# Performance work log

Hardware: AMD Instinct MI355X
Metric: run time of the kernel (lower is better)

Reference implementation:

```python
import jax, jax.numpy as jnp
import numpy as np

D = 256; R = 2; K = 32
N = 32768; NE = 1_000_000; NT = 65_536
BETA_MAX = 5.0; GRAD_CLIP = 1.0; STATE_CLIP = 10.0
DAMP = 0.9999  # update_damping=1.0 clamped to 1-1e-4
EPS = 1e-5


def _xavier(key, din, dout, gain=0.5):
    lim = gain * np.sqrt(6.0 / (din + dout))
    return jax.random.uniform(key, (din, dout), jnp.float32, -lim, lim)


def setup_inputs() -> dict:
    key = jax.random.key(0)
    ks = jax.random.split(key, 16)
    inv_sp1 = float(np.log(np.expm1(1.0)))  # inverse softplus of 1.0
    return {
        "X": jax.random.normal(ks[0], (N, D), jnp.float32),
        "c_2": jax.random.randint(ks[1], (NE,), 0, N, jnp.int32),
        "u_2": jax.random.randint(ks[2], (NE,), 0, N, jnp.int32),
        "c_3": jax.random.randint(ks[3], (NT,), 0, N, jnp.int32),
        "u_3": jax.random.randint(ks[4], (NT,), 0, N, jnp.int32),
        "v_3": jax.random.randint(ks[5], (NT,), 0, N, jnp.int32),
        "t_tau": jax.random.randint(ks[6], (NT,), 0, 2, jnp.int32),
        "step_size": jnp.float32(0.1),
        "ln_gamma": jnp.ones((D,), jnp.float32),
        "ln_beta": jnp.zeros((D,), jnp.float32),
        "W_Q2": _xavier(ks[7], D, D),
        "W_K2": _xavier(ks[8], D, D),
        "W_Q3": _xavier(ks[9], D, R * D),
        "W_K3": _xavier(ks[10], D, R * D),
        "T_tau": 0.02 * jax.random.normal(ks[11], (2, R, D), jnp.float32),
        "W_Qm": _xavier(ks[12], D, D),
        "W_Km": _xavier(ks[13], D, D),
        "B_mem": jax.random.normal(ks[14], (K, D), jnp.float32) / np.sqrt(D),
        "lambda_2": jnp.float32(inv_sp1), "lambda_3": jnp.float32(inv_sp1), "lambda_m": jnp.float32(inv_sp1),
        "beta_2": jnp.float32(inv_sp1), "beta_3": jnp.float32(inv_sp1), "beta_m": jnp.float32(inv_sp1),
    }


def _seg_lse(s, seg, n):
    # logsumexp of s grouped by seg; empty segments contribute 0
    m = jax.ops.segment_max(s, seg, num_segments=n)
    m0 = jnp.where(jnp.isfinite(m), m, 0.0)
    e = jax.ops.segment_sum(jnp.exp(s - m0[seg]), seg, num_segments=n)
    return jnp.where(e > 0, m0 + jnp.log(jnp.maximum(e, 1e-30)), 0.0)


def _energy(X, ln_gamma, ln_beta, W_Q2, W_K2, W_Q3, W_K3, T_tau, W_Qm, W_Km, B_mem,
            lambda_2, lambda_3, lambda_m, beta_2, beta_3, beta_m,
            c_2, u_2, c_3, u_3, v_3, t_tau):
    mu = X.mean(-1, keepdims=True)
    var = ((X - mu) ** 2).mean(-1, keepdims=True)
    G = (X - mu) * jax.lax.rsqrt(var + EPS) * ln_gamma + ln_beta  # [N,D]
    sp = jax.nn.softplus
    lam2, lam3, lamm = sp(lambda_2), sp(lambda_3), sp(lambda_m)
    b2 = jnp.minimum(sp(beta_2), BETA_MAX)
    b3 = jnp.minimum(sp(beta_3), BETA_MAX)
    bm = jnp.minimum(sp(beta_m), BETA_MAX)
    scale = jnp.float32(1.0 / np.sqrt(D))
    # pairwise (order-2) attention energy over edge list
    Q2, K2 = G @ W_Q2, G @ W_K2
    s2 = b2 * scale * jnp.sum(Q2[c_2] * K2[u_2], axis=-1)  # [NE]
    E2 = -(lam2 / b2) * jnp.sum(_seg_lse(s2, c_2, N))
    # motif (order-3) rank-R energy over triangle list with type embedding T_tau
    Q3 = (G @ W_Q3).reshape(N, R, D)
    K3 = (G @ W_K3).reshape(N, R, D)
    s3 = b3 * scale * jnp.sum(Q3[c_3] * K3[u_3] * K3[v_3] * T_tau[t_tau], axis=(1, 2))  # [NT]
    E3 = -(lam3 / b3) * jnp.sum(_seg_lse(s3, c_3, N))
    # memory-slot energy
    Qm, Km = G @ W_Qm, B_mem @ W_Km  # [N,D],[K,D]
    Sm = bm * scale * (Qm @ Km.T)  # [N,K]
    Em = -(lamm / bm) * jnp.sum(jax.nn.logsumexp(Sm, axis=-1))
    return E2 + E3 + Em


def reference(X, c_2, u_2, c_3, u_3, v_3, t_tau, step_size, ln_gamma, ln_beta,
              W_Q2, W_K2, W_Q3, W_K3, T_tau, W_Qm, W_Km, B_mem,
              lambda_2, lambda_3, lambda_m, beta_2, beta_3, beta_m):
    efn = lambda x: _energy(x, ln_gamma, ln_beta, W_Q2, W_K2, W_Q3, W_K3, T_tau,
                            W_Qm, W_Km, B_mem, lambda_2, lambda_3, lambda_m,
                            beta_2, beta_3, beta_m, c_2, u_2, c_3, u_3, v_3, t_tau)
    E, gX = jax.value_and_grad(efn)(X)
    gn = jnp.maximum(jnp.linalg.norm(gX, axis=-1, keepdims=True), 1e-6)
    gX = gX * jnp.minimum(GRAD_CLIP / gn, 1.0)
    X_next = X - step_size * DAMP * gX
    sn = jnp.maximum(jnp.linalg.norm(X_next, axis=-1, keepdims=True), 1e-6)
    X_next = X_next * jnp.minimum(STATE_CLIP / sn, 1.0)
    return X_next, E
```

## Files before the change

kernel.cpp:

```cpp
#include <hip/hip_runtime.h>
#include <math.h>

#define D_ 256
#define KSLOT 32
#define CAP2 128
#define CAP3C 16
#define CAP3I 32
#define NBP 256
#define NBUCK 256
typedef unsigned short ushort_t;
typedef __attribute__((ext_vector_type(8))) short bf16x8;
typedef __attribute__((ext_vector_type(4))) float f32x4;

__device__ __forceinline__ float softplus_f(float x){
  return (x > 20.0f) ? x : log1pf(expf(x));
}
__device__ __forceinline__ float bflo(unsigned u){ return __uint_as_float(u << 16); }
__device__ __forceinline__ float bfhi(unsigned u){ return __uint_as_float(u & 0xFFFF0000u); }
__device__ __forceinline__ ushort_t f2b(float f){
  unsigned u = __float_as_uint(f);
  unsigned r = u + 0x7FFFu + ((u >> 16) & 1u);
  return (ushort_t)(r >> 16);
}
__device__ __forceinline__ unsigned pack2(float a, float b){
  return (unsigned)f2b(a) | ((unsigned)f2b(b) << 16);
}
__device__ __forceinline__ void unpack16(uint4 a, uint4 b, float* f){
  f[0]=bflo(a.x); f[1]=bfhi(a.x); f[2]=bflo(a.y); f[3]=bfhi(a.y);
  f[4]=bflo(a.z); f[5]=bfhi(a.z); f[6]=bflo(a.w); f[7]=bfhi(a.w);
  f[8]=bflo(b.x); f[9]=bfhi(b.x); f[10]=bflo(b.y); f[11]=bfhi(b.y);
  f[12]=bflo(b.z); f[13]=bfhi(b.z); f[14]=bflo(b.w); f[15]=bfhi(b.w);
}
__device__ __forceinline__ float block_reduce_sum(float v, float* sbuf){
  #pragma unroll
  for (int o = 32; o > 0; o >>= 1) v += __shfl_xor(v, o);
  int t = threadIdx.x, wid = t >> 6, lane = t & 63;
  if (lane == 0) sbuf[wid] = v;
  __syncthreads();
  if (t == 0) sbuf[0] = sbuf[0] + sbuf[1] + sbuf[2] + sbuf[3];
  __syncthreads();
  float r = sbuf[0];
  __syncthreads();
  return r;
}

__global__ __launch_bounds__(256) void zerok(float4* __restrict__ p, size_t n4){
  float4 z; z.x = z.y = z.z = z.w = 0.f;
  for (size_t i = (size_t)blockIdx.x * 256 + threadIdx.x; i < n4; i += (size_t)gridDim.x * 256)
    p[i] = z;
}

__global__ __launch_bounds__(256) void ln_fwd(const float* __restrict__ X, const float* __restrict__ gamma,
    const float* __restrict__ beta, ushort_t* __restrict__ Gb, float* __restrict__ mean, float* __restrict__ rstd)
{
  __shared__ float sbuf[8];
  int n = blockIdx.x, t = threadIdx.x;
  size_t idx = (size_t)n * D_ + t;
  float x = X[idx];
  float mu = block_reduce_sum(x, sbuf) * (1.0f / D_);
  float d = x - mu;
  float var = block_reduce_sum(d * d, sbuf) * (1.0f / D_);
  float rs = rsqrtf(var + 1e-5f);
  Gb[idx] = f2b(d * rs * gamma[t] + beta[t]);
  if (t == 0){ mean[n] = mu; rstd[n] = rs; }
}

__global__ __launch_bounds__(256) void wprep_all(const float* __restrict__ W_Q2, const float* __restrict__ W_K2,
    const float* __restrict__ W_Q3, const float* __restrict__ W_K3, const float* __restrict__ W_Qm,
    ushort_t* __restrict__ WtQm, ushort_t* __restrict__ WtF2, ushort_t* __restrict__ WtF3,
    ushort_t* __restrict__ WbQm, ushort_t* __restrict__ Bt2, ushort_t* __restrict__ Bt3)
{
  int idx = blockIdx.x * 256 + threadIdx.x;
  if (idx < 65536){
    int m = idx >> 8, k = idx & 255;
    WtQm[idx] = f2b(W_Qm[k * 256 + m]);
    return;
  }
  idx -= 65536;
  if (idx < 131072){
    int m = idx >> 8, k = idx & 255;
    WtF2[idx] = f2b(m < 256 ? W_Q2[k * 256 + m] : W_K2[k * 256 + (m - 256)]);
    return;
  }
  idx -= 131072;
  if (idx < 262144){
    int m = idx >> 8, k = idx & 255;
    WtF3[idx] = f2b(m < 512 ? W_Q3[k * 512 + m] : W_K3[k * 512 + (m - 512)]);
    return;
  }
  idx -= 262144;
  if (idx < 65536){ WbQm[idx] = f2b(W_Qm[idx]); return; }
  idx -= 65536;
  if (idx < 131072){
    int d = idx >> 9, k = idx & 511;
    Bt2[idx] = f2b(k < 256 ? W_Q2[d * 256 + k] : W_K2[d * 256 + (k - 256)]);
    return;
  }
  idx -= 131072;
  if (idx < 262144){
    int d = idx >> 10, k = idx & 1023;
    Bt3[idx] = f2b(k < 512 ? W_Q3[d * 512 + k] : W_K3[d * 512 + (k - 512)]);
  }
}

template<int OUT_MODE>
__global__ __launch_bounds__(256) void gemm_bt_mfma(const ushort_t* __restrict__ A,
    const ushort_t* __restrict__ Bt, void* __restrict__ C, int K, int M)
{
  __shared__ __align__(16) ushort_t As[128 * 32];
  __shared__ __align__(16) ushort_t Bs[128 * 32];
  int t = threadIdx.x;
  int wave = t >> 6, lane = t & 63;
  int row0 = blockIdx.y * 128;
  int col0 = blockIdx.x * 128;
  int wrow = (wave & 1) * 64;
  int wcol = (wave >> 1) * 64;
  f32x4 acc[4][4];
  #pragma unroll
  for (int i = 0; i < 4; ++i)
    #pragma unroll
    for (int j = 0; j < 4; ++j)
      acc[i][j] = (f32x4){0.f, 0.f, 0.f, 0.f};
  int srow = wave * 32 + (lane >> 2);
  int skoff = (lane & 3) * 8;
  const ushort_t* Ag0 = A + (size_t)(row0 + srow) * K + skoff;
  const ushort_t* Ag1 = A + (size_t)(row0 + srow + 16) * K + skoff;
  const ushort_t* Bg0 = Bt + (size_t)(col0 + srow) * K + skoff;
  const ushort_t* Bg1 = Bt + (size_t)(col0 + srow + 16) * K + skoff;
  ushort_t* Al0 = As + wave * 1024;
  ushort_t* Al1 = As + wave * 1024 + 512;
  ushort_t* Bl0 = Bs + wave * 1024;
  ushort_t* Bl1 = Bs + wave * 1024 + 512;
  int lrow = lane & 15, lk = (lane >> 4) * 8;
  for (int k0 = 0; k0 < K; k0 += 32){
    __syncthreads();
    __builtin_amdgcn_global_load_lds((const __attribute__((address_space(1))) void*)(Ag0 + k0),
                                     (__attribute__((address_space(3))) void*)Al0, 16, 0, 0);
    __builtin_amdgcn_global_load_lds((const __attribute__((address_space(1))) void*)(Ag1 + k0),
                                     (__attribute__((address_space(3))) void*)Al1, 16, 0, 0);
    __builtin_amdgcn_global_load_lds((const __attribute__((address_space(1))) void*)(Bg0 + k0),
                                     (__attribute__((address_space(3))) void*)Bl0, 16, 0, 0);
    __builtin_amdgcn_global_load_lds((const __attribute__((address_space(1))) void*)(Bg1 + k0),
                                     (__attribute__((address_space(3))) void*)Bl1, 16, 0, 0);
    __syncthreads();
    bf16x8 af[4], bf_[4];
    #pragma unroll
    for (int i = 0; i < 4; ++i)
      af[i] = *(const bf16x8*)(As + (wrow + i * 16 + lrow) * 32 + lk);
    #pragma unroll
    for (int j = 0; j < 4; ++j)
      bf_[j] = *(const bf16x8*)(Bs + (wcol + j * 16 + lrow) * 32 + lk);
    #pragma unroll
    for (int i = 0; i < 4; ++i)
      #pragma unroll
      for (int j = 0; j < 4; ++j)
        acc[i][j] = __builtin_amdgcn_mfma_f32_16x16x32_bf16(af[i], bf_[j], acc[i][j], 0, 0, 0);
  }
  int rbase = row0 + wrow + (lane >> 4) * 4;
  int cbase = col0 + wcol + (lane & 15);
  #pragma unroll
  for (int i = 0; i < 4; ++i){
    #pragma unroll
    for (int r = 0; r < 4; ++r){
      size_t rowoff = (size_t)(rbase + i * 16 + r) * M;
      #pragma unroll
      for (int j = 0; j < 4; ++j){
        int col = cbase + j * 16;
        float v = acc[i][j][r];
        if (OUT_MODE == 0)      ((float*)C)[rowoff + col] = v;
        else if (OUT_MODE == 1) ((float*)C)[rowoff + col] += v;
        else                    ((ushort_t*)C)[rowoff + col] = f2b(v);
      }
    }
  }
}

__global__ __launch_bounds__(256) void km_kernel(const float* __restrict__ Bm, const float* __restrict__ W,
    ushort_t* __restrict__ Kmb)
{
  __shared__ float sb[D_];
  int k = blockIdx.x, t = threadIdx.x;
  if (k < KSLOT){
    sb[t] = Bm[(size_t)k * D_ + t];
    __syncthreads();
    float acc = 0.f;
    for (int d = 0; d < D_; ++d) acc += sb[d] * W[(size_t)d * D_ + t];
    Kmb[(size_t)k * D_ + t] = f2b(acc);
  } else {
    Kmb[(size_t)k * D_ + t] = 0;
  }
}

__global__ __launch_bounds__(256) void softmax32(const float* __restrict__ Sm, ushort_t* __restrict__ Pb,
    float* __restrict__ lseM, const float* __restrict__ bmp, const float* __restrict__ lmp)
{
  int t = threadIdx.x;
  int r = blockIdx.x * 8 + (t >> 5);
  int lane = t & 31;
  float bs = fminf(softplus_f(*bmp), 5.0f) * 0.0625f;
  float coef = -softplus_f(*lmp) * 0.0625f;
  float s = Sm[(size_t)r * 128 + lane] * bs;
  float m = s;
  #pragma unroll
  for (int o = 16; o > 0; o >>= 1) m = fmaxf(m, __shfl_xor(m, o, 32));
  float e = __expf(s - m);
  float se = e;
  #pragma unroll
  for (int o = 16; o > 0; o >>= 1) se += __shfl_xor(se, o, 32);
  ushort_t* dst = Pb + (size_t)r * 128 + lane;
  dst[0] = f2b(coef * e / se);
  dst[32] = 0; dst[64] = 0; dst[96] = 0;
  if (lane == 0) lseM[r] = m + logf(se);
}

__global__ __launch_bounds__(256) void p2_hist(const unsigned* __restrict__ key, int stride, int NE_, int chunk,
    unsigned* __restrict__ bh)
{
  __shared__ unsigned h[256];
  int t = threadIdx.x, b = blockIdx.x;
  h[t] = 0;
  __syncthreads();
  int s = b * chunk, e = s + chunk; if (e > NE_) e = NE_;
  for (int i = s + t; i < e; i += 256)
    atomicAdd(&h[(key[(size_t)i * stride] >> 7) & 255u], 1u);
  __syncthreads();
  bh[b * 256 + t] = h[t];
}

__global__ __launch_bounds__(256) void p2_scan(unsigned* __restrict__ bh, int nb, unsigned* __restrict__ base)
{
  __shared__ unsigned ss[256];
  int t = threadIdx.x;
  unsigned tot = 0;
  for (int b = 0; b < nb; ++b) tot += bh[b * 256 + t];
  ss[t] = tot;
  __syncthreads();
  #pragma unroll
  for (int o = 1; o < 256; o <<= 1){
    unsigned v = (t >= o) ? ss[t - o] : 0u;
    __syncthreads();
    ss[t] += v;
    __syncthreads();
  }
  unsigned excl = ss[t] - tot;
  base[t] = excl;
  if (t == 255) base[256] = ss[t];
  unsigned run = excl;
  for (int b = 0; b < nb; ++b){
    unsigned v = bh[b * 256 + t];
    bh[b * 256 + t] = run;
    run += v;
  }
}

__global__ __launch_bounds__(256) void p2_place_c(const int* __restrict__ c2, const int* __restrict__ u2,
    int NE_, int chunk, const unsigned* __restrict__ bh, unsigned* __restrict__ part)
{
  __shared__ unsigned cur[256];
  int t = threadIdx.x, b = blockIdx.x;
  cur[t] = bh[b * 256 + t];
  __syncthreads();
  int s = b * chunk, e = s + chunk; if (e > NE_) e = NE_;
  for (int i = s + t; i < e; i += 256){
    unsigned c = (unsigned)c2[i], u = (unsigned)u2[i];
    unsigned dst = atomicAdd(&cur[c >> 7], 1u);
    part[dst] = ((c & 127u) << 15) | u;
  }
}

__global__ __launch_bounds__(256) void p2_fine_c(const unsigned* __restrict__ part, const unsigned* __restrict__ base,
    ushort_t* __restrict__ adjc, int* __restrict__ cntC, uint2* __restrict__ pairsU)
{
  __shared__ unsigned cnt[128];
  __shared__ ushort_t stage[128 * 128];
  int t = threadIdx.x, b = blockIdx.x;
  if (t < 128) cnt[t] = 0;
  __syncthreads();
  int s = (int)base[b], e = (int)base[b + 1];
  for (int i = s + t; i < e; i += 256){
    unsigned w = part[i];
    unsigned r = w >> 15, u = w & 32767u;
    unsigned slot = atomicAdd(&cnt[r], 1u);
    uint2 pr;
    pr.x = u;
    if (slot < 128u){
      stage[r * 128 + slot] = (ushort_t)u;
      pr.y = (((unsigned)b * 128u + r) << 7) | slot;
    } else {
      pr.y = 0xFFFFFFFFu;
    }
    pairsU[i] = pr;
  }
  __syncthreads();
  if (t < 128) cntC[b * 128 + t] = (int)cnt[t];
  for (int i = t; i < 16384; i += 256)
    adjc[(size_t)b * 16384 + i] = stage[i];
}

__global__ __launch_bounds__(256) void p2_place_u(const uint2* __restrict__ pairs, int NE_, int chunk,
    const unsigned* __restrict__ bh, uint2* __restrict__ part)
{
  __shared__ unsigned cur[256];
  int t = threadIdx.x, b = blockIdx.x;
  cur[t] = bh[b * 256 + t];
  __syncthreads();
  int s = b * chunk, e = s + chunk; if (e > NE_) e = NE_;
  for (int i = s + t; i < e; i += 256){
    uint2 pr = pairs[i];
    unsigned dst = atomicAdd(&cur[pr.x >> 7], 1u);
    part[dst] = pr;
  }
}

__global__ __launch_bounds__(256) void p2_fine_u(const uint2* __restrict__ part, const unsigned* __restrict__ base,
    int* __restrict__ adju, int* __restrict__ cntU)
{
  __shared__ unsigned cnt[128];
  __shared__ unsigned stage[128 * 128];
  int t = threadIdx.x, b = blockIdx.x;
  if (t < 128) cnt[t] = 0;
  __syncthreads();
  int s = (int)base[b], e = (int)base[b + 1];
  for (int i = s + t; i < e; i += 256){
    uint2 pr = part[i];
    if (pr.y == 0xFFFFFFFFu) continue;
    unsigned r = pr.x & 127u;
    unsigned slot = atomicAdd(&cnt[r], 1u);
    if (slot < 128u) stage[r * 128 + slot] = pr.y;
  }
  __syncthreads();
  if (t < 128) cntU[b * 128 + t] = (int)cnt[t];
  for (int i = t; i < 16384; i += 256)
    adju[(size_t)b * 16384 + i] = (int)stage[i];
}

__global__ __launch_bounds__(256) void scatter3(const int* __restrict__ c3, const int* __restrict__ u3,
    const int* __restrict__ v3, const int* __restrict__ tt, int* __restrict__ cnt3C, int* __restrict__ cnt3I,
    unsigned* __restrict__ adj3c, uint2* __restrict__ adj3i, int NT_)
{
  int e = blockIdx.x * 256 + threadIdx.x;
  if (e >= NT_) return;
  int c = c3[e], u = u3[e], v = v3[e], tau = tt[e];
  int pc = atomicAdd(cnt3C + c, 1);
  if (pc >= CAP3C) return;
  int cslot = (c << 4) + pc;
  adj3c[cslot] = (unsigned)u | ((unsigned)v << 15) | ((unsigned)tau << 30);
  int pu = atomicAdd(cnt3I + u, 1);
  if (pu < CAP3I){
    uint2 eu; eu.x = (unsigned)c | ((unsigned)tau << 15) | ((unsigned)v << 16); eu.y = (unsigned)cslot;
    adj3i[(u << 5) + pu] = eu;
  }
  int pv = atomicAdd(cnt3I + v, 1);
  if (pv < CAP3I){
    uint2 ev; ev.x = (unsigned)c | ((unsigned)tau << 15) | ((unsigned)u << 16); ev.y = (unsigned)cslot;
    adj3i[(v << 5) + pv] = ev;
  }
}

__global__ __launch_bounds__(256) void e2_rowc(const ushort_t* __restrict__ QK2, const int* __restrict__ cntC,
    const ushort_t* __restrict__ adjc, ushort_t* __restrict__ dstage, float* __restrict__ s2e,
    float2* __restrict__ ml2, const float* __restrict__ b2p, const float* __restrict__ l2p)
{
  int wave = threadIdx.x >> 6, lane = threadIdx.x & 63;
  int r = blockIdx.x * 4 + wave;
  int quarter = lane >> 4, sub = lane & 15;
  float b2s = fminf(softplus_f(*b2p), 5.0f) * 0.0625f;
  float lam2 = softplus_f(*l2p);
  int start = r << 7;
  int deg = cntC[r]; if (deg > CAP2) deg = CAP2;
  int end = start + deg;
  const ushort_t* qrow = QK2 + (size_t)r * 512 + sub * 16;
  float qf[16];
  unpack16(*(const uint4*)qrow, *(const uint4*)(qrow + 8), qf);
  float m = -1e30f, l = 0.f;
  float a[16] = {};
  int p = start + quarter;
  uint4 k0, k1;
  if (p < end){
    const ushort_t* krow = QK2 + (size_t)adjc[p] * 512 + 256 + sub * 16;
    k0 = *(const uint4*)krow; k1 = *(const uint4*)(krow + 8);
  }
  while (p < end){
    int pn = p + 4;
    uint4 n0, n1;
    if (pn < end){
      const ushort_t* krow = QK2 + (size_t)adjc[pn] * 512 + 256 + sub * 16;
      n0 = *(const uint4*)krow; n1 = *(const uint4*)(krow + 8);
    }
    float kf[16];
    unpack16(k0, k1, kf);
    float d = 0.f;
    #pragma unroll
    for (int j = 0; j < 16; ++j) d += qf[j] * kf[j];
    d += __shfl_xor(d, 1); d += __shfl_xor(d, 2); d += __shfl_xor(d, 4); d += __shfl_xor(d, 8);
    float s = d * b2s;
    if (sub == 0) s2e[p] = s;
    if (s <= m){
      float pt = __expf(s - m);
      l += pt;
      #pragma unroll
      for (int j = 0; j < 16; ++j) a[j] += pt * kf[j];
    } else {
      float sc = __expf(m - s);
      l = l * sc + 1.0f;
      #pragma unroll
      for (int j = 0; j < 16; ++j) a[j] = a[j] * sc + kf[j];
      m = s;
    }
    k0 = n0; k1 = n1; p = pn;
  }
  float M = fmaxf(m, __shfl_xor(m, 16)); M = fmaxf(M, __shfl_xor(M, 32));
  float scq = __expf(m - M);
  float L = l * scq;
  L += __shfl_xor(L, 16); L += __shfl_xor(L, 32);
  #pragma unroll
  for (int j = 0; j < 16; ++j){
    float x = a[j] * scq;
    x += __shfl_xor(x, 16); x += __shfl_xor(x, 32);
    a[j] = x;
  }
  float linv = 0.f, coef = 0.f;
  if (deg > 0){ linv = 1.0f / L; coef = -lam2 * 0.0625f * linv; }
  if (lane == 0){
    float2 ml; ml.x = M; ml.y = linv;
    ml2[r] = ml;
  }
  if (quarter == 0){
    ushort_t* dst = dstage + (size_t)r * 512 + sub * 16;
    uint4 p0, p1;
    p0.x = pack2(coef*a[0], coef*a[1]);   p0.y = pack2(coef*a[2], coef*a[3]);
    p0.z = pack2(coef*a[4], coef*a[5]);   p0.w = pack2(coef*a[6], coef*a[7]);
    p1.x = pack2(coef*a[8], coef*a[9]);   p1.y = pack2(coef*a[10], coef*a[11]);
    p1.z = pack2(coef*a[12], coef*a[13]); p1.w = pack2(coef*a[14], coef*a[15]);
    *(uint4*)dst = p0; *(uint4*)(dst + 8) = p1;
  }
}

__global__ __launch_bounds__(256) void e2_rowu(const ushort_t* __restrict__ QK2, const int* __restrict__ cntU,
    const int* __restrict__ adju, const float* __restrict__ s2e, const float2* __restrict__ ml2,
    ushort_t* __restrict__ dstage, const float* __restrict__ l2p)
{
  int wave = threadIdx.x >> 6, lane = threadIdx.x & 63;
  int r = blockIdx.x * 4 + wave;
  int quarter = lane >> 4, sub = lane & 15;
  float lam2 = softplus_f(*l2p);
  int start = r << 7;
  int deg = cntU[r]; if (deg > CAP2) deg = CAP2;
  int end = start + deg;
  float a[16] = {};
  int p = start + quarter;
  uint4 q0a, q0b; float sv0 = 0.f; float2 mlv0 = {0.f, 0.f};
  if (p < end){
    int gs = adju[p];
    int c = gs >> 7;
    sv0 = s2e[gs]; mlv0 = ml2[c];
    const ushort_t* qrow = QK2 + (size_t)c * 512 + sub * 16;
    q0a = *(const uint4*)qrow; q0b = *(const uint4*)(qrow + 8);
  }
  while (p < end){
    int pn = p + 4;
    uint4 q1a, q1b; float sv1 = 0.f; float2 mlv1 = {0.f, 0.f};
    if (pn < end){
      int gs = adju[pn];
      int c = gs >> 7;
      sv1 = s2e[gs]; mlv1 = ml2[c];
      const ushort_t* qrow = QK2 + (size_t)c * 512 + sub * 16;
      q1a = *(const uint4*)qrow; q1b = *(const uint4*)(qrow + 8);
    }
    float pe = __expf(sv0 - mlv0.x) * mlv0.y;
    float qf[16];
    unpack16(q0a, q0b, qf);
    #pragma unroll
    for (int j = 0; j < 16; ++j) a[j] += pe * qf[j];
    q0a = q1a; q0b = q1b; sv0 = sv1; mlv0 = mlv1; p = pn;
  }
  #pragma unroll
  for (int j = 0; j < 16; ++j){
    float x = a[j];
    x += __shfl_xor(x, 16); x += __shfl_xor(x, 32);
    a[j] = x;
  }
  float coef = -lam2 * 0.0625f;
  if (quarter == 0){
    ushort_t* dst = dstage + (size_t)r * 512 + 256 + sub * 16;
    uint4 p0, p1;
    p0.x = pack2(coef*a[0], coef*a[1]);   p0.y = pack2(coef*a[2], coef*a[3]);
    p0.z = pack2(coef*a[4], coef*a[5]);   p0.w = pack2(coef*a[6], coef*a[7]);
    p1.x = pack2(coef*a[8], coef*a[9]);   p1.y = pack2(coef*a[10], coef*a[11]);
    p1.z = pack2(coef*a[12], coef*a[13]); p1.w = pack2(coef*a[14], coef*a[15]);
    *(uint4*)dst = p0; *(uint4*)(dst + 8) = p1;
  }
}

__global__ __launch_bounds__(256) void e3_rowc(const ushort_t* __restrict__ QK3, const float* __restrict__ Tt,
    const int* __restrict__ cnt3C, const unsigned* __restrict__ adj3c, ushort_t* __restrict__ dstage,
    float* __restrict__ s3c, float2* __restrict__ ml3, const float* __restrict__ b3p,
    const float* __restrict__ l3p)
{
  __shared__ float sT[1024];
  int wave = threadIdx.x >> 6, lane = threadIdx.x & 63;
  int r = blockIdx.x * 4 + wave;
  for (int i = threadIdx.x; i < 1024; i += 256) sT[i] = Tt[i];
  __syncthreads();
  float b3s = fminf(softplus_f(*b3p), 5.0f) * 0.0625f;
  float lam3 = softplus_f(*l3p);
  int start = r << 4;
  int deg = cnt3C[r]; if (deg > CAP3C) deg = CAP3C;
  int end = start + deg;
  uint4 qw = *(const uint4*)(QK3 + (size_t)r * 1024 + lane * 8);
  float q[8] = {bflo(qw.x),bfhi(qw.x),bflo(qw.y),bfhi(qw.y),bflo(qw.z),bfhi(qw.z),bflo(qw.w),bfhi(qw.w)};
  float T0[8], T1[8];
  #pragma unroll
  for (int j = 0; j < 8; ++j){ T0[j] = sT[lane * 8 + j]; T1[j] = sT[512 + lane * 8 + j]; }
  float m = -1e30f, l = 0.f;
  float a[8] = {};
  int p = start;
  unsigned ent0 = 0; uint4 bw0, cw0;
  if (p < end){
    ent0 = adj3c[p];
    int u = ent0 & 32767, v = (ent0 >> 15) & 32767;
    bw0 = *(const uint4*)(QK3 + (size_t)u * 1024 + 512 + lane * 8);
    cw0 = *(const uint4*)(QK3 + (size_t)v * 1024 + 512 + lane * 8);
  }
  while (p < end){
    int pn = p + 1;
    unsigned ent1 = 0; uint4 bw1, cw1;
    if (pn < end){
      ent1 = adj3c[pn];
      int u = ent1 & 32767, v = (ent1 >> 15) & 32767;
      bw1 = *(const uint4*)(QK3 + (size_t)u * 1024 + 512 + lane * 8);
      cw1 = *(const uint4*)(QK3 + (size_t)v * 1024 + 512 + lane * 8);
    }
    int tau = (ent0 >> 30) & 1;
    float kb[8] = {bflo(bw0.x),bfhi(bw0.x),bflo(bw0.y),bfhi(bw0.y),bflo(bw0.z),bfhi(bw0.z),bflo(bw0.w),bfhi(bw0.w)};
    float kc[8] = {bflo(cw0.x),bfhi(cw0.x),bflo(cw0.y),bfhi(cw0.y),bflo(cw0.z),bfhi(cw0.z),bflo(cw0.w),bfhi(cw0.w)};
    float prod[8];
    float d = 0.f;
    #pragma unroll
    for (int j = 0; j < 8; ++j){
      float tj = tau ? T1[j] : T0[j];
      prod[j] = kb[j] * kc[j] * tj;
      d += q[j] * prod[j];
    }
    #pragma unroll
    for (int o = 32; o > 0; o >>= 1) d += __shfl_xor(d, o);
    float s = d * b3s;
    if (lane == 0) s3c[p] = s;
    if (s <= m){
      float pt = __expf(s - m);
      l += pt;
      #pragma unroll
      for (int j = 0; j < 8; ++j) a[j] += pt * prod[j];
    } else {
      float sc = __expf(m - s);
      l = l * sc + 1.0f;
      #pragma unroll
      for (int j = 0; j < 8; ++j) a[j] = a[j] * sc + prod[j];
      m = s;
    }
    ent0 = ent1; bw0 = bw1; cw0 = cw1; p = pn;
  }
  float linv = 0.f, coef = 0.f;
  if (deg > 0){ linv = 1.0f / l; coef = -lam3 * 0.0625f * linv; }
  uint4 o4;
  o4.x = pack2(coef*a[0], coef*a[1]); o4.y = pack2(coef*a[2], coef*a[3]);
  o4.z = pack2(coef*a[4], coef*a[5]); o4.w = pack2(coef*a[6], coef*a[7]);
  *(uint4*)(dstage + (size_t)r * 1024 + lane * 8) = o4;
  if (lane == 0){
    float2 ml; ml.x = m; ml.y = linv;
    ml3[r] = ml;
  }
}

__global__ __launch_bounds__(256) void e3_rowi(const ushort_t* __restrict__ QK3, const float* __restrict__ Tt,
    const int* __restrict__ cnt3I, const uint2* __restrict__ adj3i, const float* __restrict__ s3c,
    const float2* __restrict__ ml3, ushort_t* __restrict__ dstage, const float* __restrict__ l3p)
{
  __shared__ float sT[1024];
  int wave = threadIdx.x >> 6, lane = threadIdx.x & 63;
  int r = blockIdx.x * 4 + wave;
  for (int i = threadIdx.x; i < 1024; i += 256) sT[i] = Tt[i];
  __syncthreads();
  float lam3 = softplus_f(*l3p);
  int start = r << 5;
  int deg = cnt3I[r]; if (deg > CAP3I) deg = CAP3I;
  int end = start + deg;
  float T0[8], T1[8];
  #pragma unroll
  for (int j = 0; j < 8; ++j){ T0[j] = sT[lane * 8 + j]; T1[j] = sT[512 + lane * 8 + j]; }
  float a[8] = {};
  int p = start;
  uint2 e0; uint4 qw0, ow0; float sv0 = 0.f; float2 mlv0 = {0.f, 0.f};
  if (p < end){
    e0 = adj3i[p];
    int c = e0.x & 32767, other = (e0.x >> 16) & 32767;
    sv0 = s3c[e0.y]; mlv0 = ml3[c];
    qw0 = *(const uint4*)(QK3 + (size_t)c * 1024 + lane * 8);
    ow0 = *(const uint4*)(QK3 + (size_t)other * 1024 + 512 + lane * 8);
  }
  while (p < end){
    int pn = p + 1;
    uint2 e1; uint4 qw1, ow1; float sv1 = 0.f; float2 mlv1 = {0.f, 0.f};
    if (pn < end){
      e1 = adj3i[pn];
      int c = e1.x & 32767, other = (e1.x >> 16) & 32767;
      sv1 = s3c[e1.y]; mlv1 = ml3[c];
      qw1 = *(const uint4*)(QK3 + (size_t)c * 1024 + lane * 8);
      ow1 = *(const uint4*)(QK3 + (size_t)other * 1024 + 512 + lane * 8);
    }
    int tau = (e0.x >> 15) & 1;
    float pe = __expf(sv0 - mlv0.x) * mlv0.y;
    float q[8] = {bflo(qw0.x),bfhi(qw0.x),bflo(qw0.y),bfhi(qw0.y),bflo(qw0.z),bfhi(qw0.z),bflo(qw0.w),bfhi(qw0.w)};
    float ko[8] = {bflo(ow0.x),bfhi(ow0.x),bflo(ow0.y),bfhi(ow0.y),bflo(ow0.z),bfhi(ow0.z),bflo(ow0.w),bfhi(ow0.w)};
    #pragma unroll
    for (int j = 0; j < 8; ++j){
      float tj = tau ? T1[j] : T0[j];
      a[j] += pe * q[j] * ko[j] * tj;
    }
    e0 = e1; qw0 = qw1; ow0 = ow1; sv0 = sv1; mlv0 = mlv1; p = pn;
  }
  float coef = -lam3 * 0.0625f;
  uint4 o4;
  o4.x = pack2(coef*a[0], coef*a[1]); o4.y = pack2(coef*a[2], coef*a[3]);
  o4.z = pack2(coef*a[4], coef*a[5]); o4.w = pack2(coef*a[6], coef*a[7]);
  *(uint4*)(dstage + (size_t)r * 1024 + 512 + lane * 8) = o4;
}

__global__ __launch_bounds__(256) void ln_bwd_update(const float* __restrict__ X, const float* __restrict__ dG,
    const float* __restrict__ gamma, const float* __restrict__ mean, const float* __restrict__ rstd,
    const float* __restrict__ step_p, float* __restrict__ out)
{
  __shared__ float sbuf[8];
  int n = blockIdx.x, t = threadIdx.x;
  size_t idx = (size_t)n * D_ + t;
  float x = X[idx];
  float rs = rstd[n];
  float xh = (x - mean[n]) * rs;
  float dxh = dG[idx] * gamma[t];
  float s1 = block_reduce_sum(dxh, sbuf) * (1.0f / D_);
  float s2v = block_reduce_sum(dxh * xh, sbuf) * (1.0f / D_);
  float dx = rs * (dxh - s1 - xh * s2v);
  float gn2 = block_reduce_sum(dx * dx, sbuf);
  float gn = fmaxf(sqrtf(gn2), 1e-6f);
  float gsc = fminf(1.0f / gn, 1.0f);
  float stp = step_p[0] * 0.9999f;
  float xn = x - stp * gsc * dx;
  float sn2 = block_reduce_sum(xn * xn, sbuf);
  float sn = fmaxf(sqrtf(sn2), 1e-6f);
  float ssc = fminf(10.0f / sn, 1.0f);
  out[idx] = xn * ssc;
}

__global__ __launch_bounds__(256) void energy_partial(const float2* __restrict__ ml2, const float2* __restrict__ ml3,
    const float* __restrict__ lseM, int n, float* __restrict__ eacc)
{
  __shared__ float sbuf[8];
  int t = threadIdx.x;
  float a2 = 0.f, a3 = 0.f, am = 0.f;
  for (int i = blockIdx.x * 256 + t; i < n; i += gridDim.x * 256){
    float2 v2 = ml2[i];
    if (v2.y > 0.f) a2 += v2.x - logf(v2.y);
    float2 v3 = ml3[i];
    if (v3.y > 0.f) a3 += v3.x - logf(v3.y);
    am += lseM[i];
  }
  float s2 = block_reduce_sum(a2, sbuf);
  float s3 = block_reduce_sum(a3, sbuf);
  float sm = block_reduce_sum(am, sbuf);
  if (t == 0){
    atomicAdd(eacc + 0, s2);
    atomicAdd(eacc + 1, s3);
    atomicAdd(eacc + 2, sm);
  }
}

__global__ __launch_bounds__(64) void energy_combine(const float* __restrict__ eacc,
    const float* l2p, const float* l3p, const float* lmp,
    const float* b2p, const float* b3p, const float* bmp, float* __restrict__ outE)
{
  if (threadIdx.x == 0){
    float l2 = softplus_f(*l2p), l3 = softplus_f(*l3p), lm = softplus_f(*lmp);
    float b2 = fminf(softplus_f(*b2p), 5.0f);
    float b3 = fminf(softplus_f(*b3p), 5.0f);
    float bm = fminf(softplus_f(*bmp), 5.0f);
    *outE = -(l2 / b2) * eacc[0] - (l3 / b3) * eacc[1] - (lm / bm) * eacc[2];
  }
}

static inline void zfill(void* p, size_t nElems, hipStream_t stream){
  size_t n4 = nElems / 4;
  int blocks = (int)(((n4 + 255) / 256) < 16384 ? ((n4 + 255) / 256) : 16384);
  if (blocks < 1) blocks = 1;
  zerok<<<blocks, 256, 0, stream>>>((float4*)p, n4);
}

extern "C" void kernel_launch(void* const* d_in, const int* in_sizes, int n_in,
                              void* d_out, int out_size, void* d_ws, size_t ws_size,
                              hipStream_t stream)
{
  const float* X     = (const float*)d_in[0];
  const int*   c2    = (const int*)d_in[1];
  const int*   u2    = (const int*)d_in[2];
  const int*   c3    = (const int*)d_in[3];
  const int*   u3    = (const int*)d_in[4];
  const int*   v3    = (const int*)d_in[5];
  const int*   tt    = (const int*)d_in[6];
  const float* stepp = (const float*)d_in[7];
  const float* gamma = (const float*)d_in[8];
  const float* beta  = (const float*)d_in[9];
  const float* W_Q2  = (const float*)d_in[10];
  const float* W_K2  = (const float*)d_in[11];
  const float* W_Q3  = (const float*)d_in[12];
  const float* W_K3  = (const float*)d_in[13];
  const float* T_tau = (const float*)d_in[14];
  const float* W_Qm  = (const float*)d_in[15];
  const float* W_Km  = (const float*)d_in[16];
  const float* B_mem = (const float*)d_in[17];
  const float* l2p   = (const float*)d_in[18];
  const float* l3p   = (const float*)d_in[19];
  const float* lmp   = (const float*)d_in[20];
  const float* b2p   = (const float*)d_in[21];
  const float* b3p   = (const float*)d_in[22];
  const float* bmp   = (const float*)d_in[23];

  const int N  = in_sizes[0] / D_;
  const int NE = in_sizes[1];
  const int NT = in_sizes[3];
  const size_t ND = (size_t)N * D_;

  char* base = (char*)d_ws;
  size_t off = 0;
  auto alloc = [&](size_t bytes) -> void* {
    void* p = base + off;
    off += (bytes + 255) & ~(size_t)255;
    return p;
  };
  ushort_t* Gb    = (ushort_t*)alloc(ND * 2);
  ushort_t* bufA  = (ushort_t*)alloc(ND * 4 * 2);
  ushort_t* bufB  = (ushort_t*)alloc(ND * 4 * 2);
  int*      zreg  = (int*)     alloc(((size_t)4 * N + 16) * 4);
  ushort_t* adjc  = (ushort_t*)alloc((size_t)N * CAP2 * 2);
  int*      adju  = (int*)     alloc((size_t)N * CAP2 * 4);
  unsigned* adj3c = (unsigned*)alloc((size_t)N * CAP3C * 4);
  uint2*    adj3i = (uint2*)   alloc((size_t)N * CAP3I * 8);
  float*    s3c   = (float*)   alloc((size_t)N * CAP3C * 4);
  float2*   ml2   = (float2*)  alloc((size_t)N * 8);
  float2*   ml3   = (float2*)  alloc((size_t)N * 8);
  ushort_t* Kmb   = (ushort_t*)alloc((size_t)128 * 256 * 2);
  ushort_t* KWb   = (ushort_t*)alloc((size_t)256 * 128 * 2);
  float*    meanb = (float*)   alloc((size_t)N * 4);
  float*    rstdb = (float*)   alloc((size_t)N * 4);
  float*    lseM  = (float*)   alloc((size_t)N * 4);
  ushort_t* WtQm  = (ushort_t*)alloc(65536 * 2);
  ushort_t* WtF2  = (ushort_t*)alloc(131072 * 2);
  ushort_t* WtF3  = (ushort_t*)alloc(262144 * 2);
  ushort_t* WbQm  = (ushort_t*)alloc(65536 * 2);
  ushort_t* Bt2   = (ushort_t*)alloc(131072 * 2);
  ushort_t* Bt3   = (ushort_t*)alloc(262144 * 2);

  int* cntC  = zreg;
  int* cntU  = zreg + N;
  int* cnt3C = zreg + 2 * N;
  int* cnt3I = zreg + 3 * N;
  float* eacc = (float*)(zreg + 4 * N);
  float* out = (float*)d_out;
  float*    Sm  = (float*)bufB;
  ushort_t* Pb  = (ushort_t*)(Sm + (size_t)N * 128);
  float*    s2e = (float*)(bufB + ND * 2);

  unsigned* partA  = (unsigned*)bufA;
  uint2*    pairsU = (uint2*)((char*)bufA + ((size_t)8 << 20));
  unsigned* bhC    = (unsigned*)((char*)bufA + ((size_t)16 << 20));
  unsigned* bhU    = bhC + NBP * 256;
  unsigned* baseC  = bhU + NBP * 256;
  unsigned* baseU  = baseC + 512;

  zfill(zreg, (size_t)4 * N + 16, stream);

  ln_fwd<<<N, 256, 0, stream>>>(X, gamma, beta, Gb, meanb, rstdb);
  wprep_all<<<(917504 + 255) / 256, 256, 0, stream>>>(W_Q2, W_K2, W_Q3, W_K3, W_Qm,
      WtQm, WtF2, WtF3, WbQm, Bt2, Bt3);

  {
    int chunk = (NE + NBP - 1) / NBP;
    p2_hist<<<NBP, 256, 0, stream>>>((const unsigned*)c2, 1, NE, chunk, bhC);
    p2_scan<<<1, 256, 0, stream>>>(bhC, NBP, baseC);
    p2_place_c<<<NBP, 256, 0, stream>>>(c2, u2, NE, chunk, bhC, partA);
    p2_fine_c<<<NBUCK, 256, 0, stream>>>(partA, baseC, adjc, cntC, pairsU);
    p2_hist<<<NBP, 256, 0, stream>>>((const unsigned*)pairsU, 2, NE, chunk, bhU);
    p2_scan<<<1, 256, 0, stream>>>(bhU, NBP, baseU);
    p2_place_u<<<NBP, 256, 0, stream>>>(pairsU, NE, chunk, bhU, (uint2*)partA);
    p2_fine_u<<<NBUCK, 256, 0, stream>>>((const uint2*)partA, baseU, adju, cntU);
  }
  scatter3<<<(NT + 255) / 256, 256, 0, stream>>>(c3, u3, v3, tt, cnt3C, cnt3I, adj3c, adj3i, NT);

  dim3 g256(2, N / 128), g512(4, N / 128), g1024(8, N / 128);

  km_kernel<<<128, 256, 0, stream>>>(B_mem, W_Km, Kmb);
  gemm_bt_mfma<2><<<dim3(1, 2), 256, 0, stream>>>(WbQm, Kmb, KWb, 256, 128);
  gemm_bt_mfma<2><<<g256, 256, 0, stream>>>(Gb, WtQm, bufA, D_, D_);
  gemm_bt_mfma<0><<<dim3(1, N / 128), 256, 0, stream>>>(bufA, Kmb, Sm, 256, 128);
  softmax32<<<N / 8, 256, 0, stream>>>(Sm, Pb, lseM, bmp, lmp);
  gemm_bt_mfma<0><<<g256, 256, 0, stream>>>(Pb, KWb, out, 128, D_);

  gemm_bt_mfma<2><<<g512, 256, 0, stream>>>(Gb, WtF2, bufA, D_, 512);
  e2_rowc<<<N / 4, 256, 0, stream>>>(bufA, cntC, adjc, bufB, s2e, ml2, b2p, l2p);
  e2_rowu<<<N / 4, 256, 0, stream>>>(bufA, cntU, adju, s2e, ml2, bufB, l2p);
  gemm_bt_mfma<1><<<g256, 256, 0, stream>>>(bufB, Bt2, out, 512, D_);

  gemm_bt_mfma<2><<<g1024, 256, 0, stream>>>(Gb, WtF3, bufA, D_, 1024);
  e3_rowc<<<N / 4, 256, 0, stream>>>(bufA, T_tau, cnt3C, adj3c, bufB, s3c, ml3, b3p, l3p);
  e3_rowi<<<N / 4, 256, 0, stream>>>(bufA, T_tau, cnt3I, adj3i, s3c, ml3, bufB, l3p);
  gemm_bt_mfma<1><<<g256, 256, 0, stream>>>(bufB, Bt3, out, 1024, D_);

  ln_bwd_update<<<N, 256, 0, stream>>>(X, out, gamma, meanb, rstdb, stepp, out);

  energy_partial<<<128, 256, 0, stream>>>(ml2, ml3, lseM, N, eacc);
  energy_combine<<<1, 64, 0, stream>>>(eacc, l2p, l3p, lmp, b2p, b3p, bmp, out + ND);
}
```

Baseline: 839.9 us.

## Sort adjacency rows in LDS to make CSR build deterministic and gather-friendly

Inside the two fine-bucketing kernels, each adjacency row staged in LDS is insertion-sorted by one thread per row. The pairs array for the second pass is rewritten in sorted row order, and overflow entries are compacted at the end. The aim is deterministic adjacency ordering and better locality for the later gathers over neighbours. In exchange, the insertion sort is serial per row (up to 128 entries, quadratic cost) and half the threads sit idle, which lengthens these kernels. The padded row stride of 130 may also change LDS bank behaviour.

```diff
diff --git a/kernel.cpp b/kernel.cpp
--- a/kernel.cpp
+++ b/kernel.cpp
@@ -272,29 +272,60 @@
     ushort_t* __restrict__ adjc, int* __restrict__ cntC, uint2* __restrict__ pairsU)
 {
   __shared__ unsigned cnt[128];
-  __shared__ ushort_t stage[128 * 128];
+  __shared__ unsigned rowoff[128];
+  __shared__ unsigned ovfU[128];
+  __shared__ unsigned ovfCnt;
+  __shared__ ushort_t stage[128 * 130];
   int t = threadIdx.x, b = blockIdx.x;
   if (t < 128) cnt[t] = 0;
+  if (t == 0) ovfCnt = 0;
   __syncthreads();
   int s = (int)base[b], e = (int)base[b + 1];
   for (int i = s + t; i < e; i += 256){
     unsigned w = part[i];
     unsigned r = w >> 15, u = w & 32767u;
     unsigned slot = atomicAdd(&cnt[r], 1u);
-    uint2 pr;
-    pr.x = u;
-    if (slot < 128u){
-      stage[r * 128 + slot] = (ushort_t)u;
-      pr.y = (((unsigned)b * 128u + r) << 7) | slot;
-    } else {
-      pr.y = 0xFFFFFFFFu;
-    }
-    pairsU[i] = pr;
-  }
-  __syncthreads();
-  if (t < 128) cntC[b * 128 + t] = (int)cnt[t];
-  for (int i = t; i < 16384; i += 256)
-    adjc[(size_t)b * 16384 + i] = stage[i];
+    if (slot < 128u) stage[r * 130 + slot] = (ushort_t)u;
+    else { unsigned di = atomicAdd(&ovfCnt, 1u); if (di < 128u) ovfU[di] = u; }
+  }
+  __syncthreads();
+  if (t < 128){
+    unsigned c_ = cnt[t]; if (c_ > 128u) c_ = 128u; cnt[t] = c_;
+    ushort_t* row = stage + t * 130;
+    for (unsigned k = 1; k < c_; ++k){
+      ushort_t key = row[k];
+      int j = (int)k - 1;
+      while (j >= 0 && row[j] > key){ row[j + 1] = row[j]; --j; }
+      row[j + 1] = key;
+    }
+    cntC[b * 128 + t] = (int)c_;
+  }
+  __syncthreads();
+  if (t == 0){
+    unsigned run = 0;
+    for (int r = 0; r < 128; ++r){ rowoff[r] = run; run += cnt[r]; }
+  }
+  __syncthreads();
+  if (t < 128){
+    unsigned c_ = cnt[t];
+    unsigned base0 = (unsigned)s + rowoff[t];
+    unsigned gsbase = (((unsigned)b * 128u + (unsigned)t) << 7);
+    for (unsigned k = 0; k < c_; ++k){
+      uint2 pr; pr.x = (unsigned)stage[t * 130 + k]; pr.y = gsbase | k;
+      pairsU[base0 + k] = pr;
+    }
+  }
+  __syncthreads();
+  unsigned kept = rowoff[127] + cnt[127];
+  unsigned ovfT = ovfCnt;
+  for (unsigned d = t; d < ovfT; d += 256){
+    uint2 pr; pr.x = (d < 128u) ? ovfU[d] : 0u; pr.y = 0xFFFFFFFFu;
+    pairsU[s + kept + d] = pr;
+  }
+  for (int i = t; i < 16384; i += 256){
+    int r = i >> 7, k2 = i & 127;
+    adjc[(size_t)b * 16384 + i] = stage[r * 130 + k2];
+  }
 }
 
 __global__ __launch_bounds__(256) void p2_place_u(const uint2* __restrict__ pairs, int NE_, int chunk,
@@ -316,7 +347,7 @@
     int* __restrict__ adju, int* __restrict__ cntU)
 {
   __shared__ unsigned cnt[128];
-  __shared__ unsigned stage[128 * 128];
+  __shared__ unsigned stage[128 * 130];
   int t = threadIdx.x, b = blockIdx.x;
   if (t < 128) cnt[t] = 0;
   __syncthreads();
@@ -326,12 +357,25 @@
     if (pr.y == 0xFFFFFFFFu) continue;
     unsigned r = pr.x & 127u;
     unsigned slot = atomicAdd(&cnt[r], 1u);
-    if (slot < 128u) stage[r * 128 + slot] = pr.y;
-  }
-  __syncthreads();
-  if (t < 128) cntU[b * 128 + t] = (int)cnt[t];
-  for (int i = t; i < 16384; i += 256)
-    adju[(size_t)b * 16384 + i] = (int)stage[i];
+    if (slot < 128u) stage[r * 130 + slot] = pr.y;
+  }
+  __syncthreads();
+  if (t < 128){
+    unsigned c_ = cnt[t]; if (c_ > 128u) c_ = 128u;
+    unsigned* row = stage + t * 130;
+    for (unsigned k = 1; k < c_; ++k){
+      unsigned key = row[k];
+      int j = (int)k - 1;
+      while (j >= 0 && row[j] > key){ row[j + 1] = row[j]; --j; }
+      row[j + 1] = key;
+    }
+    cntU[b * 128 + t] = (int)c_;
+  }
+  __syncthreads();
+  for (int i = t; i < 16384; i += 256){
+    int r = i >> 7, k2 = i & 127;
+    adju[(size_t)b * 16384 + i] = (int)stage[r * 130 + k2];
+  }
 }
 
 __global__ __launch_bounds__(256) void scatter3(const int* __restrict__ c3, const int* __restrict__ u3,
```

Result: slower. 963.3 us (+14.7%).
